# Kernel tuning notes

Measured on AMD Instinct MI355X. Metric: run time of the kernel, lower is better.

Reference implementation:

```python
import jax, jax.numpy as jnp
import numpy as np

D = 1024      # d_model
H = 16        # n_head
DK = 64       # d_k = d_v
NL = 4        # n_layers
DFF = 4096    # d_inner
ROT = 32      # rotary dim = max((d_word_vec//n_head)//2, 32)
BASE = 4096.0
EPS = 1e-6
B, L = 2, 1024


def setup_inputs() -> dict:
    key = jax.random.key(0)
    ks = jax.random.split(key, 16)
    s = 0.02
    return {
        "src_seq": jax.random.normal(ks[0], (B, L, D), dtype=jnp.float32),
        "Wq": jax.random.normal(ks[1], (NL, D, H * DK), dtype=jnp.float32) * s,
        "Wk": jax.random.normal(ks[2], (NL, D, H * DK), dtype=jnp.float32) * s,
        "Wv": jax.random.normal(ks[3], (NL, D, H * DK), dtype=jnp.float32) * s,
        "Wo": jax.random.normal(ks[4], (NL, H * DK, D), dtype=jnp.float32) * s,
        "ln1_g": jnp.ones((NL, D), dtype=jnp.float32),
        "ln1_b": jnp.zeros((NL, D), dtype=jnp.float32),
        "W1": jax.random.normal(ks[5], (NL, D, DFF), dtype=jnp.float32) * s,
        "b1": jnp.zeros((NL, DFF), dtype=jnp.float32),
        "W2": jax.random.normal(ks[6], (NL, DFF, D), dtype=jnp.float32) * s,
        "b2": jnp.zeros((NL, D), dtype=jnp.float32),
        "ln2_g": jnp.ones((NL, D), dtype=jnp.float32),
        "ln2_b": jnp.zeros((NL, D), dtype=jnp.float32),
        "ln0_g": jnp.ones((D,), dtype=jnp.float32),
        "ln0_b": jnp.zeros((D,), dtype=jnp.float32),
    }


def _layer_norm(x, g, b):
    mu = jnp.mean(x, axis=-1, keepdims=True)
    var = jnp.mean(jnp.square(x - mu), axis=-1, keepdims=True)
    return (x - mu) * jax.lax.rsqrt(var + EPS) * g + b


def _rope_tables(seq_len):
    # RotaryEmbedding: inv_freq over rotary dim ROT, positions 0..L-1, freqs duplicated.
    inv_freq = 1.0 / (BASE ** (jnp.arange(0, ROT, 2, dtype=jnp.float32) / ROT))
    freqs = jnp.arange(seq_len, dtype=jnp.float32)[:, None] * inv_freq  # [L, ROT/2]
    freqs = jnp.concatenate([freqs, freqs], axis=-1)                     # [L, ROT]
    # Faithful quirk: apply_rotary_pos_emb sees t as [B,L,H,dk] so seq_len=H there,
    # hence freqs[-H:] of shape [H,ROT] broadcasts over the HEAD axis.
    fr = freqs[-H:]
    return jnp.cos(fr), jnp.sin(fr)  # each [H, ROT]


def _apply_rope(t, cos, sin):
    # t: [B, L, H, DK]; rotate first ROT dims, pass the rest through.
    tr, tu = t[..., :ROT], t[..., ROT:]
    x = tr.reshape(*tr.shape[:-1], 2, ROT // 2)
    rot = jnp.concatenate([-x[..., 1, :], x[..., 0, :]], axis=-1)
    return jnp.concatenate([tr * cos + rot * sin, tu], axis=-1)


def reference(src_seq, Wq, Wk, Wv, Wo, ln1_g, ln1_b, W1, b1, W2, b2,
              ln2_g, ln2_b, ln0_g, ln0_b):
    b, l, _ = src_seq.shape
    cos, sin = _rope_tables(l)
    inv_temp = 1.0 / jnp.sqrt(jnp.float32(DK))

    x = src_seq * jnp.sqrt(jnp.float32(D))   # scale_emb
    x = _layer_norm(x, ln0_g, ln0_b)         # pre-stack layer norm

    def step(x, p):
        wq, wk, wv, wo, g1, be1, w1, c1, w2, c2, g2, be2 = p
        q = (x @ wq).reshape(b, l, H, DK)
        k = (x @ wk).reshape(b, l, H, DK)
        v = (x @ wv).reshape(b, l, H, DK)
        q = _apply_rope(q, cos, sin)
        k = _apply_rope(k, cos, sin)
        scores = jnp.einsum('blhd,bmhd->bhlm', q * inv_temp, k)
        attn = jax.nn.softmax(scores, axis=-1)
        o = jnp.einsum('bhlm,bmhd->blhd', attn, v).reshape(b, l, H * DK)
        x1 = _layer_norm(o @ wo + x, g1, be1)
        h = jax.nn.relu(x1 @ w1 + c1)
        x2 = _layer_norm(h @ w2 + c2 + x1, g2, be2)
        return x2, None

    x, _ = jax.lax.scan(step, x, (Wq, Wk, Wv, Wo, ln1_g, ln1_b, W1, b1, W2, b2, ln2_g, ln2_b))
    return x
```

## Files before the change

### kernel.cpp

```cpp
#include <hip/hip_runtime.h>
#include <hip/hip_bf16.h>
#include <cstdint>
#include <cstddef>

typedef __bf16 bf16_t;
typedef __bf16 bf16x8 __attribute__((ext_vector_type(8)));
typedef __bf16 bf16x4 __attribute__((ext_vector_type(4)));
typedef float  f32x4  __attribute__((ext_vector_type(4)));

#define DEV __device__ __forceinline__

DEV void gload16(void* lds, const void* gmem) {
  __builtin_amdgcn_global_load_lds(
      (const __attribute__((address_space(1))) void*)gmem,
      (__attribute__((address_space(3))) void*)lds, 16, 0, 0);
}

DEV f32x4 mfma16(bf16x8 a, bf16x8 b, f32x4 c) {
  return __builtin_amdgcn_mfma_f32_16x16x32_bf16(a, b, c, 0, 0, 0);
}

__global__ __launch_bounds__(256)
void conv_t_kernel(const float* __restrict__ src, bf16_t* __restrict__ dst,
                   int K, int N) {
  __shared__ float tile[64][65];
  const int k0 = blockIdx.x * 64, n0 = blockIdx.y * 64;
  const int t = threadIdx.x;
#pragma unroll
  for (int c = 0; c < 16; c++) {
    int idx = c * 256 + t;
    int r = idx >> 6, cc = idx & 63;
    tile[r][cc] = src[(size_t)(k0 + r) * N + n0 + cc];
  }
  __syncthreads();
#pragma unroll
  for (int c = 0; c < 16; c++) {
    int idx = c * 256 + t;
    int r = idx >> 6, cc = idx & 63;
    dst[(size_t)(n0 + r) * K + k0 + cc] = (bf16_t)tile[cc][r];
  }
}

__global__ __launch_bounds__(256)
void conv4_kernel(const float* __restrict__ w0, const float* __restrict__ w1,
                  const float* __restrict__ w2, const float* __restrict__ w3,
                  bf16_t* __restrict__ d0, bf16_t* __restrict__ d1,
                  bf16_t* __restrict__ d2, bf16_t* __restrict__ d3) {
  const float* src = (blockIdx.z == 0) ? w0 : (blockIdx.z == 1) ? w1
                     : (blockIdx.z == 2) ? w2 : w3;
  bf16_t* dst = (blockIdx.z == 0) ? d0 : (blockIdx.z == 1) ? d1
                : (blockIdx.z == 2) ? d2 : d3;
  __shared__ float tile[64][65];
  const int k0 = blockIdx.x * 64, n0 = blockIdx.y * 64;
  const int t = threadIdx.x;
#pragma unroll
  for (int c = 0; c < 16; c++) {
    int idx = c * 256 + t;
    int r = idx >> 6, cc = idx & 63;
    tile[r][cc] = src[(size_t)(k0 + r) * 1024 + n0 + cc];
  }
  __syncthreads();
#pragma unroll
  for (int c = 0; c < 16; c++) {
    int idx = c * 256 + t;
    int r = idx >> 6, cc = idx & 63;
    dst[(size_t)(n0 + r) * 1024 + k0 + cc] = (bf16_t)tile[cc][r];
  }
}

__global__ __launch_bounds__(256)
void ln_kernel(const float* __restrict__ in, const float* __restrict__ resid,
               const float* __restrict__ g, const float* __restrict__ bt,
               float alpha, float* __restrict__ outf, bf16_t* __restrict__ outb) {
  const int row = blockIdx.x, t = threadIdx.x;
  const float4 vi = *(const float4*)(in + (size_t)row * 1024 + t * 4);
  float x0 = vi.x * alpha, x1 = vi.y * alpha, x2 = vi.z * alpha, x3 = vi.w * alpha;
  if (resid) {
    const float4 rv = *(const float4*)(resid + (size_t)row * 1024 + t * 4);
    x0 += rv.x; x1 += rv.y; x2 += rv.z; x3 += rv.w;
  }
  float s = x0 + x1 + x2 + x3;
  float sq = x0 * x0 + x1 * x1 + x2 * x2 + x3 * x3;
#pragma unroll
  for (int m = 1; m < 64; m <<= 1) { s += __shfl_xor(s, m); sq += __shfl_xor(sq, m); }
  __shared__ float ps[4], pq[4];
  const int wave = t >> 6;
  if ((t & 63) == 0) { ps[wave] = s; pq[wave] = sq; }
  __syncthreads();
  s = ps[0] + ps[1] + ps[2] + ps[3];
  sq = pq[0] + pq[1] + pq[2] + pq[3];
  const float mu = s * (1.0f / 1024.0f);
  const float var = sq * (1.0f / 1024.0f) - mu * mu;
  const float rs = rsqrtf(var + 1e-6f);
  const float4 gv = *(const float4*)(g + t * 4);
  const float4 bv = *(const float4*)(bt + t * 4);
  float y0 = (x0 - mu) * rs * gv.x + bv.x;
  float y1 = (x1 - mu) * rs * gv.y + bv.y;
  float y2 = (x2 - mu) * rs * gv.z + bv.z;
  float y3 = (x3 - mu) * rs * gv.w + bv.w;
  if (outf) *(float4*)(outf + (size_t)row * 1024 + t * 4) = make_float4(y0, y1, y2, y3);
  if (outb) {
    bf16x4 o; o[0] = (bf16_t)y0; o[1] = (bf16_t)y1; o[2] = (bf16_t)y2; o[3] = (bf16_t)y3;
    *(bf16x4*)(outb + (size_t)row * 1024 + t * 4) = o;
  }
}

template <int EPI>
__global__ __launch_bounds__(256, 2)
void gemm128(const bf16_t* __restrict__ A, const bf16_t* __restrict__ Bt,
             const float* __restrict__ bias, float* __restrict__ Cf,
             bf16_t* __restrict__ Cb, int N, int K, int KL) {
  constexpr int BM = 128, BN = 128, BK = 64;
  __shared__ __align__(16) bf16_t As[2][BM * BK];
  __shared__ __align__(16) bf16_t Bs[2][BN * BK];
  const int tid = threadIdx.x;
  const int wave = tid >> 6, lane = tid & 63;
  const int l16 = lane & 15, l4 = lane >> 4;
  const int m0 = blockIdx.x * BM, n0 = blockIdx.y * BN;
  const int wm = wave >> 1, wn = wave & 1;
  const int kbase = blockIdx.z * KL;
  f32x4 acc[4][4] = {};

  const int nt = KL / BK;
  auto stage = [&](int buf, int k0) {
#pragma unroll
    for (int c = 0; c < 4; c++) {
      int gidx = c * 256 + tid;
      int row = gidx >> 3, s = gidx & 7;
      gload16(&As[buf][(c * 256 + wave * 64) * 8],
              A + (size_t)(m0 + row) * K + kbase + k0 + ((s ^ (row & 7)) << 3));
    }
#pragma unroll
    for (int c = 0; c < 4; c++) {
      int gidx = c * 256 + tid;
      int row = gidx >> 3, s = gidx & 7;
      gload16(&Bs[buf][(c * 256 + wave * 64) * 8],
              Bt + (size_t)(n0 + row) * K + kbase + k0 + ((s ^ (row & 7)) << 3));
    }
  };

  stage(0, 0);
  __syncthreads();
  for (int t = 0; t < nt; t++) {
    const int cur = t & 1;
    if (t + 1 < nt) stage(cur ^ 1, (t + 1) * BK);
    const bf16_t* as = As[cur];
    const bf16_t* bs = Bs[cur];
#pragma unroll
    for (int kk = 0; kk < 2; kk++) {
      bf16x8 af[4], bfr[4];
#pragma unroll
      for (int m = 0; m < 4; m++) {
        int row = wm * 64 + m * 16 + l16;
        af[m] = *(const bf16x8*)(as + row * 64 + ((((kk << 2) + l4) ^ (row & 7)) << 3));
      }
#pragma unroll
      for (int n = 0; n < 4; n++) {
        int row = wn * 64 + n * 16 + l16;
        bfr[n] = *(const bf16x8*)(bs + row * 64 + ((((kk << 2) + l4) ^ (row & 7)) << 3));
      }
#pragma unroll
      for (int m = 0; m < 4; m++)
#pragma unroll
        for (int n = 0; n < 4; n++)
          acc[m][n] = mfma16(af[m], bfr[n], acc[m][n]);
    }
    __syncthreads();
  }

#pragma unroll
  for (int m = 0; m < 4; m++) {
#pragma unroll
    for (int n = 0; n < 4; n++) {
      int col = n0 + wn * 64 + n * 16 + l16;
      float bv = (EPI == 1) ? bias[col] : 0.0f;
#pragma unroll
      for (int r = 0; r < 4; r++) {
        int row = m0 + wm * 64 + m * 16 + l4 * 4 + r;
        float v = acc[m][n][r] + bv;
        if (EPI == 1) {
          v = fmaxf(v, 0.0f);
          Cb[(size_t)row * N + col] = (bf16_t)v;
        } else if (EPI == 3) {
          Cf[(size_t)blockIdx.z * 2048 * N + (size_t)row * N + col] = v;
        } else {
          Cf[(size_t)row * N + col] = v;
        }
      }
    }
  }
}

__global__ __launch_bounds__(256)
void reduce_kernel(const float* __restrict__ parts, const float* __restrict__ bias,
                   float* __restrict__ out, int S) {
  const int row = blockIdx.x, c4 = threadIdx.x * 4;
  f32x4 a = *(const f32x4*)(parts + (size_t)row * 1024 + c4);
  for (int s = 1; s < S; s++)
    a += *(const f32x4*)(parts + (size_t)s * 2048 * 1024 + (size_t)row * 1024 + c4);
  if (bias) a += *(const f32x4*)(bias + c4);
  *(f32x4*)(out + (size_t)row * 1024 + c4) = a;
}

__global__ __launch_bounds__(256)
void rope_kernel(const float* __restrict__ qkv, bf16_t* __restrict__ Qb,
                 bf16_t* __restrict__ Kb) {
  const int m = blockIdx.x, t = threadIdx.x;
  const int h = t >> 4, i = t & 15;
  const int b = m >> 10, l = m & 1023;
  const float pos = (float)(1008 + h);
  const float ang = pos * exp2f(-0.75f * (float)i);
  float sn, cs;
  sincosf(ang, &sn, &cs);
  const float* q = qkv + (size_t)m * 3072 + h * 64;
  const float* k = q + 1024;
  const size_t ob = ((size_t)(b * 16 + h) * 1024 + l) * 64;
  const float it = 0.125f;
  float qi = q[i], qj = q[i + 16];
  Qb[ob + i]      = (bf16_t)((qi * cs - qj * sn) * it);
  Qb[ob + i + 16] = (bf16_t)((qj * cs + qi * sn) * it);
  Qb[ob + i + 32] = (bf16_t)(q[i + 32] * it);
  Qb[ob + i + 48] = (bf16_t)(q[i + 48] * it);
  float ki = k[i], kj = k[i + 16];
  Kb[ob + i]      = (bf16_t)(ki * cs - kj * sn);
  Kb[ob + i + 16] = (bf16_t)(kj * cs + ki * sn);
  Kb[ob + i + 32] = (bf16_t)k[i + 32];
  Kb[ob + i + 48] = (bf16_t)k[i + 48];
}

__global__ __launch_bounds__(256)
void vtrans_kernel(const float* __restrict__ qkv, bf16_t* __restrict__ Vt) {
  const int bh = blockIdx.x, lt = blockIdx.y;
  const int b = bh >> 4, h = bh & 15;
  __shared__ float tile[64][65];
  const int t = threadIdx.x;
#pragma unroll
  for (int c = 0; c < 16; c++) {
    int idx = c * 256 + t;
    int r = idx >> 6, d = idx & 63;
    tile[r][d] = qkv[(size_t)(b * 1024 + lt * 64 + r) * 3072 + 2048 + h * 64 + d];
  }
  __syncthreads();
#pragma unroll
  for (int c = 0; c < 16; c++) {
    int idx = c * 256 + t;
    int d = idx >> 6, r = idx & 63;
    Vt[((size_t)bh * 64 + d) * 1024 + lt * 64 + r] = (bf16_t)tile[r][d];
  }
}

__global__ __launch_bounds__(512, 2)
void attn_kernel(const bf16_t* __restrict__ Qb, const bf16_t* __restrict__ Kb,
                 const bf16_t* __restrict__ Vt, bf16_t* __restrict__ Ob) {
  const int bh = blockIdx.x;
  const int q0 = blockIdx.y * 64;
  const int wave = threadIdx.x >> 6, lane = threadIdx.x & 63;
  const int l16 = lane & 15, l4 = lane >> 4;
  const int qw = wave & 3, kh = wave >> 2;
  const bf16_t* Q = Qb + (size_t)bh * 65536;
  const bf16_t* K = Kb + (size_t)bh * 65536;
  const bf16_t* V = Vt + (size_t)bh * 65536;
  __shared__ __align__(16) bf16_t Plds[8][16 * 64];
  __shared__ float Olds[4][16][68];
  __shared__ float mlds[4][16], llds[4][16];
  bf16_t* pl = Plds[wave];

  const int qrow = q0 + qw * 16 + l16;
  const bf16x8 qf0 = *(const bf16x8*)(Q + (size_t)qrow * 64 + l4 * 8);
  const bf16x8 qf1 = *(const bf16x8*)(Q + (size_t)qrow * 64 + 32 + l4 * 8);

  f32x4 o[4] = {};
  float mrow[4] = {-1e30f, -1e30f, -1e30f, -1e30f};
  float lrow[4] = {0.f, 0.f, 0.f, 0.f};
  constexpr float L2E = 1.44269504088896340736f;

  for (int kt = 0; kt < 8; kt++) {
    const int j0 = (kh << 9) + kt * 64;
    f32x4 s[4] = {};
#pragma unroll
    for (int nf = 0; nf < 4; nf++) {
      const bf16_t* kp = K + (size_t)(j0 + nf * 16 + l16) * 64;
      bf16x8 k0 = *(const bf16x8*)(kp + l4 * 8);
      bf16x8 k1 = *(const bf16x8*)(kp + 32 + l4 * 8);
      s[nf] = mfma16(qf0, k0, s[nf]);
      s[nf] = mfma16(qf1, k1, s[nf]);
    }
#pragma unroll
    for (int r = 0; r < 4; r++) {
      float tm = fmaxf(fmaxf(s[0][r], s[1][r]), fmaxf(s[2][r], s[3][r]));
      tm = fmaxf(tm, __shfl_xor(tm, 1));
      tm = fmaxf(tm, __shfl_xor(tm, 2));
      tm = fmaxf(tm, __shfl_xor(tm, 4));
      tm = fmaxf(tm, __shfl_xor(tm, 8));
      const float mnew = fmaxf(mrow[r], tm);
      const float c = exp2f((mrow[r] - mnew) * L2E);
      mrow[r] = mnew;
      lrow[r] *= c;
      o[0][r] *= c; o[1][r] *= c; o[2][r] *= c; o[3][r] *= c;
      const int prow = l4 * 4 + r;
      const int rs = prow & 7;
#pragma unroll
      for (int nf = 0; nf < 4; nf++) {
        float p = exp2f((s[nf][r] - mnew) * L2E);
        lrow[r] += p;
        int gran = (nf << 1) + (l16 >> 3);
        pl[(prow << 6) + ((gran ^ rs) << 3) + (l16 & 7)] = (bf16_t)p;
      }
    }
#pragma unroll
    for (int jc = 0; jc < 2; jc++) {
      const int prow = l16;
      bf16x8 pf = *(const bf16x8*)(pl + (prow << 6) +
                                   ((((jc << 2) + l4) ^ (prow & 7)) << 3));
#pragma unroll
      for (int df = 0; df < 4; df++) {
        bf16x8 vf = *(const bf16x8*)(V + (size_t)(df * 16 + l16) * 1024 + j0 +
                                     jc * 32 + l4 * 8);
        o[df] = mfma16(pf, vf, o[df]);
      }
    }
  }

#pragma unroll
  for (int r = 0; r < 4; r++) {
    float lr = lrow[r];
    lr += __shfl_xor(lr, 1);
    lr += __shfl_xor(lr, 2);
    lr += __shfl_xor(lr, 4);
    lr += __shfl_xor(lr, 8);
    lrow[r] = lr;
  }

  if (kh == 1) {
#pragma unroll
    for (int r = 0; r < 4; r++) {
      if (l16 == 0) {
        mlds[qw][l4 * 4 + r] = mrow[r];
        llds[qw][l4 * 4 + r] = lrow[r];
      }
#pragma unroll
      for (int df = 0; df < 4; df++)
        Olds[qw][l4 * 4 + r][df * 16 + l16] = o[df][r];
    }
  }
  __syncthreads();
  if (kh == 0) {
    const int b = bh >> 4, h = bh & 15;
    float sa[4], sb[4];
#pragma unroll
    for (int r = 0; r < 4; r++) {
      const int rowl = l4 * 4 + r;
      const float pm = mlds[qw][rowl], pll = llds[qw][rowl];
      const float mn = fmaxf(mrow[r], pm);
      const float a = exp2f((mrow[r] - mn) * L2E);
      const float bsc = exp2f((pm - mn) * L2E);
      const float inv = 1.0f / (lrow[r] * a + pll * bsc);
      sa[r] = a * inv; sb[r] = bsc * inv;
    }
#pragma unroll
    for (int df = 0; df < 4; df++) {
#pragma unroll
      for (int r = 0; r < 4; r++) {
        const int rowl = l4 * 4 + r;
        const int rl = q0 + qw * 16 + rowl;
        const float v = o[df][r] * sa[r] + Olds[qw][rowl][df * 16 + l16] * sb[r];
        Ob[((size_t)(b * 1024 + rl)) * 1024 + h * 64 + df * 16 + l16] = (bf16_t)v;
      }
    }
  }
}

extern "C" void kernel_launch(void* const* d_in, const int* in_sizes, int n_in,
                              void* d_out, int out_size, void* d_ws, size_t ws_size,
                              hipStream_t stream) {
  (void)in_sizes; (void)n_in; (void)out_size;
  const float* src  = (const float*)d_in[0];
  const float* Wq   = (const float*)d_in[1];
  const float* Wk   = (const float*)d_in[2];
  const float* Wv   = (const float*)d_in[3];
  const float* Wo   = (const float*)d_in[4];
  const float* ln1g = (const float*)d_in[5];
  const float* ln1b = (const float*)d_in[6];
  const float* W1   = (const float*)d_in[7];
  const float* b1   = (const float*)d_in[8];
  const float* W2   = (const float*)d_in[9];
  const float* b2   = (const float*)d_in[10];
  const float* ln2g = (const float*)d_in[11];
  const float* ln2b = (const float*)d_in[12];
  const float* ln0g = (const float*)d_in[13];
  const float* ln0b = (const float*)d_in[14];

  char* ws = (char*)d_ws;
  size_t off = 0;
  auto alloc = [&](size_t bytes) -> char* {
    char* p = ws + off;
    off += (bytes + 255) & ~(size_t)255;
    return p;
  };
  bf16_t* wqkvt = (bf16_t*)alloc((size_t)3072 * 1024 * 2);
  bf16_t* wot   = (bf16_t*)alloc((size_t)1024 * 1024 * 2);
  bf16_t* w1t   = (bf16_t*)alloc((size_t)4096 * 1024 * 2);
  bf16_t* w2t   = (bf16_t*)alloc((size_t)1024 * 4096 * 2);
  float*  x     = (float*) alloc((size_t)2048 * 1024 * 4);
  bf16_t* xb    = (bf16_t*)alloc((size_t)2048 * 1024 * 2);
  float*  x1    = (float*) alloc((size_t)2048 * 1024 * 4);
  bf16_t* x1b   = (bf16_t*)alloc((size_t)2048 * 1024 * 2);
  float*  t0    = (float*) alloc((size_t)2048 * 1024 * 4);
  char*   R     = alloc((size_t)48 * 1024 * 1024);
  float*  qkv   = (float*)R;
  bf16_t* Qbuf  = (bf16_t*)(R + (size_t)24 * 1024 * 1024);
  bf16_t* Kbuf  = (bf16_t*)(R + (size_t)28 * 1024 * 1024);
  bf16_t* Vt    = (bf16_t*)(R + (size_t)32 * 1024 * 1024);
  bf16_t* Ob    = (bf16_t*)(R + (size_t)36 * 1024 * 1024);
  float*  parts = (float*)R;
  bf16_t* hb    = (bf16_t*)(R + (size_t)32 * 1024 * 1024);
  if (off > ws_size) return;

  ln_kernel<<<2048, 256, 0, stream>>>(src, nullptr, ln0g, ln0b, 32.0f, x, xb);

  for (int l = 0; l < 4; l++) {
    const float* wq = Wq + (size_t)l * 1024 * 1024;
    const float* wk = Wk + (size_t)l * 1024 * 1024;
    const float* wv = Wv + (size_t)l * 1024 * 1024;
    const float* wo = Wo + (size_t)l * 1024 * 1024;
    const float* w1 = W1 + (size_t)l * 1024 * 4096;
    const float* w2 = W2 + (size_t)l * 4096 * 1024;

    conv4_kernel<<<dim3(16, 16, 4), 256, 0, stream>>>(
        wq, wk, wv, wo, wqkvt, wqkvt + (size_t)1024 * 1024,
        wqkvt + (size_t)2048 * 1024, wot);
    conv_t_kernel<<<dim3(16, 64), 256, 0, stream>>>(w1, w1t, 1024, 4096);
    conv_t_kernel<<<dim3(64, 16), 256, 0, stream>>>(w2, w2t, 4096, 1024);

    gemm128<0><<<dim3(16, 24, 1), 256, 0, stream>>>(xb, wqkvt, nullptr, qkv, nullptr,
                                                    3072, 1024, 1024);
    rope_kernel<<<2048, 256, 0, stream>>>(qkv, Qbuf, Kbuf);
    vtrans_kernel<<<dim3(32, 16), 256, 0, stream>>>(qkv, Vt);
    attn_kernel<<<dim3(32, 16), 512, 0, stream>>>(Qbuf, Kbuf, Vt, Ob);

    gemm128<3><<<dim3(16, 8, 2), 256, 0, stream>>>(Ob, wot, nullptr, parts, nullptr,
                                                   1024, 1024, 512);
    reduce_kernel<<<2048, 256, 0, stream>>>(parts, nullptr, t0, 2);
    ln_kernel<<<2048, 256, 0, stream>>>(t0, x, ln1g + (size_t)l * 1024,
                                        ln1b + (size_t)l * 1024, 1.0f, x1, x1b);

    gemm128<1><<<dim3(16, 32, 1), 256, 0, stream>>>(x1b, w1t, b1 + (size_t)l * 4096,
                                                    nullptr, hb, 4096, 1024, 1024);
    gemm128<3><<<dim3(16, 8, 4), 256, 0, stream>>>(hb, w2t, nullptr, parts, nullptr,
                                                   1024, 4096, 1024);
    reduce_kernel<<<2048, 256, 0, stream>>>(parts, b2 + (size_t)l * 1024, t0, 4);

    const bool last = (l == 3);
    ln_kernel<<<2048, 256, 0, stream>>>(t0, x1, ln2g + (size_t)l * 1024,
                                        ln2b + (size_t)l * 1024, 1.0f,
                                        last ? (float*)d_out : x,
                                        last ? nullptr : xb);
  }
}
```

Before: 789.8 us.

## Rewrite attention with 32x32 MFMA, register-resident P and lazy rescaling

The attention kernel moves from 16x16x32 to 32x32x16 bf16 MFMA and computes S transposed (K as the A operand), so each lane owns one query row. P is packed to bf16 and exchanged between half-waves with shuffles instead of going through LDS. The log2(e) factor is folded into the Q scale in the rope kernel, and the running max is only updated when it grows by more than 8 (lazy rescale). Blocks shrink from 512 to 256 threads, so each wave covers 32 query rows. The lazy threshold allows intermediate exp values up to 2^8, which bf16 and fp32 handle but which slightly changes rounding behaviour.

New measurement: 689.7 us. 12.7% less time.

```diff
diff --git a/kernel.cpp b/kernel.cpp
--- a/kernel.cpp
+++ b/kernel.cpp
@@ -7,6 +7,7 @@
 typedef __bf16 bf16x8 __attribute__((ext_vector_type(8)));
 typedef __bf16 bf16x4 __attribute__((ext_vector_type(4)));
 typedef float  f32x4  __attribute__((ext_vector_type(4)));
+typedef float  f32x16 __attribute__((ext_vector_type(16)));
 
 #define DEV __device__ __forceinline__
 
@@ -18,6 +19,15 @@
 
 DEV f32x4 mfma16(bf16x8 a, bf16x8 b, f32x4 c) {
   return __builtin_amdgcn_mfma_f32_16x16x32_bf16(a, b, c, 0, 0, 0);
+}
+DEV f32x16 mfma32(bf16x8 a, bf16x8 b, f32x16 c) {
+  return __builtin_amdgcn_mfma_f32_32x32x16_bf16(a, b, c, 0, 0, 0);
+}
+
+DEV uint32_t pkbf(float a, float b) {
+  union { bf16_t h; uint16_t u; } ua, ub;
+  ua.h = (bf16_t)a; ub.h = (bf16_t)b;
+  return (uint32_t)ua.u | ((uint32_t)ub.u << 16);
 }
 
 __global__ __launch_bounds__(256)
@@ -215,7 +225,7 @@
   const float* q = qkv + (size_t)m * 3072 + h * 64;
   const float* k = q + 1024;
   const size_t ob = ((size_t)(b * 16 + h) * 1024 + l) * 64;
-  const float it = 0.125f;
+  const float it = 0.125f * 1.44269504088896340736f;
   float qi = q[i], qj = q[i + 16];
   Qb[ob + i]      = (bf16_t)((qi * cs - qj * sn) * it);
   Qb[ob + i + 16] = (bf16_t)((qj * cs + qi * sn) * it);
@@ -249,123 +259,111 @@
   }
 }
 
-__global__ __launch_bounds__(512, 2)
+__global__ __launch_bounds__(256, 2)
 void attn_kernel(const bf16_t* __restrict__ Qb, const bf16_t* __restrict__ Kb,
                  const bf16_t* __restrict__ Vt, bf16_t* __restrict__ Ob) {
   const int bh = blockIdx.x;
-  const int q0 = blockIdx.y * 64;
   const int wave = threadIdx.x >> 6, lane = threadIdx.x & 63;
-  const int l16 = lane & 15, l4 = lane >> 4;
-  const int qw = wave & 3, kh = wave >> 2;
+  const int l31 = lane & 31, hi = lane >> 5;
+  const int qt = wave & 1, kh = wave >> 1;
+  const int q0 = blockIdx.y * 64 + qt * 32;
   const bf16_t* Q = Qb + (size_t)bh * 65536;
   const bf16_t* K = Kb + (size_t)bh * 65536;
   const bf16_t* V = Vt + (size_t)bh * 65536;
-  __shared__ __align__(16) bf16_t Plds[8][16 * 64];
-  __shared__ float Olds[4][16][68];
-  __shared__ float mlds[4][16], llds[4][16];
-  bf16_t* pl = Plds[wave];
-
-  const int qrow = q0 + qw * 16 + l16;
-  const bf16x8 qf0 = *(const bf16x8*)(Q + (size_t)qrow * 64 + l4 * 8);
-  const bf16x8 qf1 = *(const bf16x8*)(Q + (size_t)qrow * 64 + 32 + l4 * 8);
-
-  f32x4 o[4] = {};
-  float mrow[4] = {-1e30f, -1e30f, -1e30f, -1e30f};
-  float lrow[4] = {0.f, 0.f, 0.f, 0.f};
-  constexpr float L2E = 1.44269504088896340736f;
-
-  for (int kt = 0; kt < 8; kt++) {
-    const int j0 = (kh << 9) + kt * 64;
-    f32x4 s[4] = {};
-#pragma unroll
-    for (int nf = 0; nf < 4; nf++) {
-      const bf16_t* kp = K + (size_t)(j0 + nf * 16 + l16) * 64;
-      bf16x8 k0 = *(const bf16x8*)(kp + l4 * 8);
-      bf16x8 k1 = *(const bf16x8*)(kp + 32 + l4 * 8);
-      s[nf] = mfma16(qf0, k0, s[nf]);
-      s[nf] = mfma16(qf1, k1, s[nf]);
-    }
-#pragma unroll
-    for (int r = 0; r < 4; r++) {
-      float tm = fmaxf(fmaxf(s[0][r], s[1][r]), fmaxf(s[2][r], s[3][r]));
-      tm = fmaxf(tm, __shfl_xor(tm, 1));
-      tm = fmaxf(tm, __shfl_xor(tm, 2));
-      tm = fmaxf(tm, __shfl_xor(tm, 4));
-      tm = fmaxf(tm, __shfl_xor(tm, 8));
-      const float mnew = fmaxf(mrow[r], tm);
-      const float c = exp2f((mrow[r] - mnew) * L2E);
-      mrow[r] = mnew;
-      lrow[r] *= c;
-      o[0][r] *= c; o[1][r] *= c; o[2][r] *= c; o[3][r] *= c;
-      const int prow = l4 * 4 + r;
-      const int rs = prow & 7;
-#pragma unroll
-      for (int nf = 0; nf < 4; nf++) {
-        float p = exp2f((s[nf][r] - mnew) * L2E);
-        lrow[r] += p;
-        int gran = (nf << 1) + (l16 >> 3);
-        pl[(prow << 6) + ((gran ^ rs) << 3) + (l16 & 7)] = (bf16_t)p;
+
+  __shared__ float Olds[2][64][32];
+  __shared__ float mlds[2][32], llds[2][32];
+
+  bf16x8 qf[4];
+#pragma unroll
+  for (int ks = 0; ks < 4; ks++)
+    qf[ks] = *(const bf16x8*)(Q + (size_t)(q0 + l31) * 64 + ks * 16 + hi * 8);
+
+  f32x16 o0 = {}, o1 = {};
+  float m2 = -1e30f, l2 = 0.0f;
+
+  union U8 { uint32_t w[4]; bf16x8 v; };
+
+  for (int kt = 0; kt < 16; kt++) {
+    const int j0 = (kh << 9) + kt * 32;
+    f32x16 st = {};
+#pragma unroll
+    for (int ks = 0; ks < 4; ks++) {
+      bf16x8 kf = *(const bf16x8*)(K + (size_t)(j0 + l31) * 64 + ks * 16 + hi * 8);
+      st = mfma32(kf, qf[ks], st);
+    }
+    float a0 = fmaxf(st[0], st[1]),  a1 = fmaxf(st[2], st[3]);
+    float a2 = fmaxf(st[4], st[5]),  a3 = fmaxf(st[6], st[7]);
+    float a4 = fmaxf(st[8], st[9]),  a5 = fmaxf(st[10], st[11]);
+    float a6 = fmaxf(st[12], st[13]), a7 = fmaxf(st[14], st[15]);
+    float tm = fmaxf(fmaxf(fmaxf(a0, a1), fmaxf(a2, a3)),
+                     fmaxf(fmaxf(a4, a5), fmaxf(a6, a7)));
+    tm = fmaxf(tm, __shfl_xor(tm, 32));
+    if (!__all(tm - m2 <= 8.0f)) {
+      const float mnew = fmaxf(m2, tm);
+      const float c = exp2f(m2 - mnew);
+      m2 = mnew;
+      l2 *= c;
+#pragma unroll
+      for (int r = 0; r < 16; r++) { o0[r] *= c; o1[r] *= c; }
+    }
+    float p[16];
+    float ls = 0.0f;
+#pragma unroll
+    for (int r = 0; r < 16; r++) { p[r] = exp2f(st[r] - m2); ls += p[r]; }
+    ls += __shfl_xor(ls, 32);
+    l2 += ls;
+    uint32_t w0 = pkbf(p[0], p[1]),   w1 = pkbf(p[2], p[3]);
+    uint32_t w2 = pkbf(p[4], p[5]),   w3 = pkbf(p[6], p[7]);
+    uint32_t w4 = pkbf(p[8], p[9]),   w5 = pkbf(p[10], p[11]);
+    uint32_t w6 = pkbf(p[12], p[13]), w7 = pkbf(p[14], p[15]);
+    uint32_t s0 = (uint32_t)__shfl_xor((int)(hi ? w0 : w2), 32);
+    uint32_t s1 = (uint32_t)__shfl_xor((int)(hi ? w1 : w3), 32);
+    uint32_t s2 = (uint32_t)__shfl_xor((int)(hi ? w4 : w6), 32);
+    uint32_t s3 = (uint32_t)__shfl_xor((int)(hi ? w5 : w7), 32);
+    U8 f0, f1;
+    f0.w[0] = hi ? s0 : w0;  f0.w[1] = hi ? s1 : w1;
+    f0.w[2] = hi ? w2 : s0;  f0.w[3] = hi ? w3 : s1;
+    f1.w[0] = hi ? s2 : w4;  f1.w[1] = hi ? s3 : w5;
+    f1.w[2] = hi ? w6 : s2;  f1.w[3] = hi ? w7 : s3;
+    const bf16_t* vp0 = V + (size_t)l31 * 1024 + j0 + hi * 8;
+    const bf16_t* vp1 = V + (size_t)(32 + l31) * 1024 + j0 + hi * 8;
+    o0 = mfma32(*(const bf16x8*)(vp0), f0.v, o0);
+    o0 = mfma32(*(const bf16x8*)(vp0 + 16), f1.v, o0);
+    o1 = mfma32(*(const bf16x8*)(vp1), f0.v, o1);
+    o1 = mfma32(*(const bf16x8*)(vp1 + 16), f1.v, o1);
+  }
+
+  if (kh == 1) {
+    if (hi == 0) { mlds[qt][l31] = m2; llds[qt][l31] = l2; }
+#pragma unroll
+    for (int r = 0; r < 16; r++) {
+      const int d = (r & 3) + 8 * (r >> 2) + 4 * hi;
+      Olds[qt][d][l31] = o0[r];
+      Olds[qt][32 + d][l31] = o1[r];
+    }
+  }
+  __syncthreads();
+  if (kh == 0) {
+    const float pm = mlds[qt][l31], pl = llds[qt][l31];
+    const float mn = fmaxf(m2, pm);
+    const float ca = exp2f(m2 - mn), cb = exp2f(pm - mn);
+    const float inv = 1.0f / (l2 * ca + pl * cb);
+    const float fa = ca * inv, fb = cb * inv;
+    const int b = bh >> 4, h = bh & 15;
+    bf16_t* op = Ob + ((size_t)(b * 1024 + q0 + l31)) * 1024 + h * 64;
+#pragma unroll
+    for (int rg = 0; rg < 4; rg++) {
+      bf16x4 v0, v1;
+#pragma unroll
+      for (int rr = 0; rr < 4; rr++) {
+        const int r = rg * 4 + rr;
+        const int d = rr + 8 * rg + 4 * hi;
+        v0[rr] = (bf16_t)(o0[r] * fa + Olds[qt][d][l31] * fb);
+        v1[rr] = (bf16_t)(o1[r] * fa + Olds[qt][32 + d][l31] * fb);
       }
-    }
-#pragma unroll
-    for (int jc = 0; jc < 2; jc++) {
-      const int prow = l16;
-      bf16x8 pf = *(const bf16x8*)(pl + (prow << 6) +
-                                   ((((jc << 2) + l4) ^ (prow & 7)) << 3));
-#pragma unroll
-      for (int df = 0; df < 4; df++) {
-        bf16x8 vf = *(const bf16x8*)(V + (size_t)(df * 16 + l16) * 1024 + j0 +
-                                     jc * 32 + l4 * 8);
-        o[df] = mfma16(pf, vf, o[df]);
-      }
-    }
-  }
-
-#pragma unroll
-  for (int r = 0; r < 4; r++) {
-    float lr = lrow[r];
-    lr += __shfl_xor(lr, 1);
-    lr += __shfl_xor(lr, 2);
-    lr += __shfl_xor(lr, 4);
-    lr += __shfl_xor(lr, 8);
-    lrow[r] = lr;
-  }
-
-  if (kh == 1) {
-#pragma unroll
-    for (int r = 0; r < 4; r++) {
-      if (l16 == 0) {
-        mlds[qw][l4 * 4 + r] = mrow[r];
-        llds[qw][l4 * 4 + r] = lrow[r];
-      }
-#pragma unroll
-      for (int df = 0; df < 4; df++)
-        Olds[qw][l4 * 4 + r][df * 16 + l16] = o[df][r];
-    }
-  }
-  __syncthreads();
-  if (kh == 0) {
-    const int b = bh >> 4, h = bh & 15;
-    float sa[4], sb[4];
-#pragma unroll
-    for (int r = 0; r < 4; r++) {
-      const int rowl = l4 * 4 + r;
-      const float pm = mlds[qw][rowl], pll = llds[qw][rowl];
-      const float mn = fmaxf(mrow[r], pm);
-      const float a = exp2f((mrow[r] - mn) * L2E);
-      const float bsc = exp2f((pm - mn) * L2E);
-      const float inv = 1.0f / (lrow[r] * a + pll * bsc);
-      sa[r] = a * inv; sb[r] = bsc * inv;
-    }
-#pragma unroll
-    for (int df = 0; df < 4; df++) {
-#pragma unroll
-      for (int r = 0; r < 4; r++) {
-        const int rowl = l4 * 4 + r;
-        const int rl = q0 + qw * 16 + rowl;
-        const float v = o[df][r] * sa[r] + Olds[qw][rowl][df * 16 + l16] * sb[r];
-        Ob[((size_t)(b * 1024 + rl)) * 1024 + h * 64 + df * 16 + l16] = (bf16_t)v;
-      }
+      *(bf16x4*)(op + 8 * rg + 4 * hi) = v0;
+      *(bf16x4*)(op + 32 + 8 * rg + 4 * hi) = v1;
     }
   }
 }
@@ -436,7 +434,7 @@
                                                     3072, 1024, 1024);
     rope_kernel<<<2048, 256, 0, stream>>>(qkv, Qbuf, Kbuf);
     vtrans_kernel<<<dim3(32, 16), 256, 0, stream>>>(qkv, Vt);
-    attn_kernel<<<dim3(32, 16), 512, 0, stream>>>(Qbuf, Kbuf, Vt, Ob);
+    attn_kernel<<<dim3(32, 16), 256, 0, stream>>>(Qbuf, Kbuf, Vt, Ob);
 
     gemm128<3><<<dim3(16, 8, 2), 256, 0, stream>>>(Ob, wot, nullptr, parts, nullptr,
                                                    1024, 1024, 512);
```
